# Performance work log

Hardware: AMD Instinct MI355X
Metric: run time of the kernel (lower is better)

## Reference

```python
import jax, jax.numpy as jnp
import numpy as np

N_NODES = 20000
K_RING = 8          # node i connects to i+1..i+K (mod n) -> degree 2K, E = N*K
D = 128
MH = 256


def _build_graph():
    n, k = N_NODES, K_RING
    i = np.arange(n, dtype=np.int64)
    # edges: eid = (j-1)*n + i  corresponds to edge (i, (i+j) % n)
    us, vs = [], []
    for j in range(1, k + 1):
        us.append(i)
        vs.append((i + j) % n)
    edges = np.stack([np.concatenate(us), np.concatenate(vs)], axis=1)  # [E,2]
    # triangle incidences: node t = (i+o)%n is adjacent to both endpoints of
    # edge (i, i+j) iff o in [j-k, k], o not in {0, j}
    tn, te = [], []
    for j in range(1, k + 1):
        eid = (j - 1) * n + i
        for o in range(j - k, k + 1):
            if o == 0 or o == j:
                continue
            tn.append((i + o) % n)
            te.append(eid)
    tri_node = np.concatenate(tn)  # [T], T = n * 84 for k=8
    tri_eid = np.concatenate(te)
    return edges, tri_node, tri_eid


def setup_inputs() -> dict:
    key = jax.random.key(0)
    ks = jax.random.split(key, 10)
    edges, tri_node, tri_eid = _build_graph()

    def w(k_, shape):
        fan_in = shape[0]
        return jax.random.normal(k_, shape, dtype=jnp.float32) * (1.0 / np.sqrt(fan_in))

    return {
        "h": jax.random.normal(ks[0], (N_NODES, D), dtype=jnp.float32),
        "edges": jnp.asarray(edges),
        "tri_node": jnp.asarray(tri_node),
        "tri_eid": jnp.asarray(tri_eid),
        "W_e1": w(ks[1], (D, MH)), "b_e1": jnp.zeros((MH,), jnp.float32),
        "W_e2": w(ks[2], (MH, D)), "b_e2": jnp.zeros((D,), jnp.float32),
        "W_f1": w(ks[3], (2 * D, MH)), "b_f1": jnp.zeros((MH,), jnp.float32),
        "W_f2": w(ks[4], (MH, D)), "b_f2": jnp.zeros((D,), jnp.float32),
        "W_r": w(ks[5], (D, D)), "b_r": jnp.zeros((D,), jnp.float32),
        "W_p1": w(ks[6], (D, MH)), "b_p1": jnp.zeros((MH,), jnp.float32),
        "W_p2": w(ks[7], (MH, D)), "b_p2": jnp.zeros((D,), jnp.float32),
    }


def _mlp(x, W1, b1, W2, b2):
    # 2-layer MLP, ReLU, dropout in eval mode (identity)
    return jnp.maximum(x @ W1 + b1, 0.0) @ W2 + b2


def reference(h, edges, tri_node, tri_eid,
              W_e1, b_e1, W_e2, b_e2,
              W_f1, b_f1, W_f2, b_f2,
              W_r, b_r, W_p1, b_p1, W_p2, b_p2):
    n = h.shape[0]
    u, v = edges[:, 0], edges[:, 1]
    h_e = _mlp(h[u] + h[v], W_e1, b_e1, W_e2, b_e2)          # [E,d]
    # aggr_t[t] = sum of h_e over edges incident to t
    ends = jnp.concatenate([u, v])
    aggr_t = jax.ops.segment_sum(jnp.concatenate([h_e, h_e], axis=0), ends,
                                 num_segments=n)               # [n,d]
    # aggr_n[t] = sum of h_e[eid] over neighbor-pair edges (triangles at t)
    aggr_n = jax.ops.segment_sum(h_e[tri_eid], tri_node, num_segments=n)
    z = _mlp(jnp.concatenate([aggr_t, aggr_n], axis=-1), W_f1, b_f1, W_f2, b_f2)
    deg = jax.ops.segment_sum(jnp.ones(ends.shape[0], h.dtype), ends,
                              num_segments=n)
    z = jnp.where((deg == 0)[:, None], 0.0, z)                 # isolated nodes
    h_new = _mlp(h @ W_r + b_r + z, W_p1, b_p1, W_p2, b_p2)    # lgan-res
    return h_new
```

## Files before the change

kernel.cpp:

```cpp
#include <hip/hip_runtime.h>


#define NN 20000
#define NE 160000
#define DD 128
#define MHD 256

typedef __attribute__((ext_vector_type(8))) short short8;
typedef __attribute__((ext_vector_type(4))) short short4v;
typedef __attribute__((ext_vector_type(4))) float f32x4;

#define SWZ(row) (((row) & 7) << 3)

__device__ __forceinline__ float bf2f(short s) {
  return __builtin_bit_cast(float, (unsigned int)((unsigned short)s) << 16);
}
__device__ __forceinline__ short f2bf(float f) {
  unsigned int u = __builtin_bit_cast(unsigned int, f);
  u = (u + 0x7FFFu + ((u >> 16) & 1u)) >> 16;
  return (short)u;
}
__device__ __forceinline__ short8 zero8() {
  short8 z;
#pragma unroll
  for (int q = 0; q < 8; ++q) z[q] = 0;
  return z;
}

#define MFMA(a, b, c) __builtin_amdgcn_mfma_f32_16x16x32_bf16((a), (b), (c), 0, 0, 0)

__global__ __launch_bounds__(256) void g_gemm(
    const short* __restrict__ hbf, const short* __restrict__ wqA,
    short* __restrict__ G) {
  __shared__ __align__(16) short WS[8192];
  const int t = threadIdx.x;
  const int lane = t & 63, w = t >> 6;
  const int lr = lane & 15, lg = lane >> 4;
  const int rbase = blockIdx.x * 128 + w * 32;

  short8 xf[2][4];
#pragma unroll
  for (int rs = 0; rs < 2; ++rs) {
    int r = rbase + rs * 16 + lr;
    if (r >= NN) r = NN - 1;
    const short* hr = hbf + (size_t)r * DD;
#pragma unroll
    for (int kk = 0; kk < 4; ++kk)
      xf[rs][kk] = *(const short8*)&hr[kk * 32 + lg * 8];
  }

#pragma unroll 1
  for (int p = 0; p < 4; ++p) {
    {
      short8 stg[4];
#pragma unroll
      for (int c = 0; c < 4; ++c)
        stg[c] = *(const short8*)&wqA[p * 8192 + (c * 256 + t) * 8];
#pragma unroll
      for (int c = 0; c < 4; ++c) *(short8*)&WS[(c * 256 + t) * 8] = stg[c];
    }
    __syncthreads();
#pragma unroll
    for (int ct = 0; ct < 4; ++ct) {
      short8 aw[4];
#pragma unroll
      for (int kk = 0; kk < 4; ++kk)
        aw[kk] = *(const short8*)&WS[(ct * 16 + lr) * 128 +
                                     (((kk * 4 + lg) ^ lr) << 3)];
#pragma unroll
      for (int rs = 0; rs < 2; ++rs) {
        f32x4 a1 = {0.f, 0.f, 0.f, 0.f};
#pragma unroll
        for (int kk = 0; kk < 4; ++kk) a1 = MFMA(aw[kk], xf[rs][kk], a1);
        const int row = rbase + rs * 16 + lr;
        if (row < NN) {
          short4v o;
#pragma unroll
          for (int q = 0; q < 4; ++q) o[q] = f2bf(a1[q]);
          const int off = p * 64 + ct * 16 + 4 * lg;
          *(short4v*)&G[(size_t)row * 256 + off] = o;
        }
      }
    }
    __syncthreads();
  }
}

#define LOADU(K, ridx)                                              \
  {                                                                 \
    int r_ = (ridx);                                                \
    if (r_ < 0) r_ += NN;                                           \
    else if (r_ >= NN) r_ -= NN;                                    \
    u##K = bf2f(G[(size_t)r_ * 256 + dbase]);                       \
  }

#define WIN(K)                                                          \
  ((K) == 0    ? u0                                                     \
   : (K) == 1  ? u1                                                     \
   : (K) == 2  ? u2                                                     \
   : (K) == 3  ? u3                                                     \
   : (K) == 4  ? u4                                                     \
   : (K) == 5  ? u5                                                     \
   : (K) == 6  ? u6                                                     \
   : (K) == 7  ? u7                                                     \
   : (K) == 8  ? u8                                                     \
   : (K) == 9  ? u9                                                     \
   : (K) == 10 ? u10                                                    \
   : (K) == 11 ? u11                                                    \
   : (K) == 12 ? u12                                                    \
   : (K) == 13 ? u13                                                    \
   : (K) == 14 ? u14                                                    \
   : (K) == 15 ? u15                                                    \
   : (K) == 16 ? u16                                                    \
   : (K) == 17 ? u17                                                    \
   : (K) == 18 ? u18                                                    \
   : (K) == 19 ? u19                                                    \
   : (K) == 20 ? u20                                                    \
   : (K) == 21 ? u21                                                    \
   : (K) == 22 ? u22                                                    \
   : (K) == 23 ? u23                                                    \
   : (K) == 24 ? u24                                                    \
   : (K) == 25 ? u25                                                    \
   : (K) == 26 ? u26                                                    \
   : (K) == 27 ? u27                                                    \
   : (K) == 28 ? u28                                                    \
   : (K) == 29 ? u29                                                    \
   : (K) == 30 ? u30                                                    \
   : (K) == 31 ? u31                                                    \
   : (K) == 32 ? u32                                                    \
   : (K) == 33 ? u33                                                    \
   : (K) == 34 ? u34                                                    \
   : (K) == 35 ? u35                                                    \
   : (K) == 36 ? u36                                                    \
   : (K) == 37 ? u37                                                    \
                : u38)

#define ADD16(base, W, v_)                                              \
  {                                                                     \
    constexpr int W__ = (W);                                            \
    if constexpr (W__ == 0) base##0 += (v_);                            \
    else if constexpr (W__ == 1) base##1 += (v_);                       \
    else if constexpr (W__ == 2) base##2 += (v_);                       \
    else if constexpr (W__ == 3) base##3 += (v_);                       \
    else if constexpr (W__ == 4) base##4 += (v_);                       \
    else if constexpr (W__ == 5) base##5 += (v_);                       \
    else if constexpr (W__ == 6) base##6 += (v_);                       \
    else if constexpr (W__ == 7) base##7 += (v_);                       \
    else if constexpr (W__ == 8) base##8 += (v_);                       \
    else if constexpr (W__ == 9) base##9 += (v_);                       \
    else if constexpr (W__ == 10) base##10 += (v_);                     \
    else if constexpr (W__ == 11) base##11 += (v_);                     \
    else if constexpr (W__ == 12) base##12 += (v_);                     \
    else if constexpr (W__ == 13) base##13 += (v_);                     \
    else if constexpr (W__ == 14) base##14 += (v_);                     \
    else if constexpr (W__ == 15) base##15 += (v_);                     \
  }

#define QJ(ii, j)                                                       \
  {                                                                     \
    float p = fmaxf(WIN((ii) + (j)) + gib, 0.f);                        \
    Q += p;                                                             \
    ADD16(sa, (ii) - 8 + (j), p)                                        \
    if constexpr ((j) <= 7) ADD16(sf, (ii) - 16 + (j), Q)               \
  }

#define PSTEP(ii)                                                       \
  {                                                                     \
    const float gib = WIN(ii) + b1v;                                    \
    float Q = 0.f;                                                      \
    QJ(ii, 1) QJ(ii, 2) QJ(ii, 3) QJ(ii, 4)                             \
    QJ(ii, 5) QJ(ii, 6) QJ(ii, 7) QJ(ii, 8)                             \
    ADD16(sa, (ii) - 8, Q)                                              \
    ADD16(sf, (ii) - 8, Q) ADD16(sf, (ii) - 7, Q) ADD16(sf, (ii) - 6, Q)\
    ADD16(sf, (ii) - 5, Q) ADD16(sf, (ii) - 4, Q) ADD16(sf, (ii) - 3, Q)\
    ADD16(sf, (ii) - 2, Q) ADD16(sf, (ii) - 1, Q) ADD16(sf, (ii) - 0, Q)\
  }

#define STORE_W(w_, saV, sfV)                                           \
  {                                                                     \
    SA[(size_t)(nb + (w_)) * 256 + sb] = f2bf(saV);                     \
    Dout[(size_t)(nb + (w_)) * 256 + sb] = f2bf(sfV - saV);             \
  }

__global__ __launch_bounds__(256) void paccum(
    const short* __restrict__ G, const float* __restrict__ be1,
    short* __restrict__ SA, short* __restrict__ Dout) {
  const int t = threadIdx.x;
  const int l = t & 63, wid = t >> 6;
  const int nb = blockIdx.x * 16;
  const int dbase = wid * 64 + l;
  const float b1v = be1[dbase];

  float u0, u1, u2, u3, u4, u5, u6, u7, u8, u9, u10, u11, u12, u13, u14,
      u15, u16, u17, u18, u19, u20, u21, u22, u23, u24, u25, u26, u27, u28,
      u29, u30, u31, u32, u33, u34, u35, u36, u37, u38;
  LOADU(0, nb - 8)  LOADU(1, nb - 7)  LOADU(2, nb - 6)  LOADU(3, nb - 5)
  LOADU(4, nb - 4)  LOADU(5, nb - 3)  LOADU(6, nb - 2)  LOADU(7, nb - 1)
  LOADU(8, nb)      LOADU(9, nb + 1)  LOADU(10, nb + 2) LOADU(11, nb + 3)
  LOADU(12, nb + 4) LOADU(13, nb + 5) LOADU(14, nb + 6) LOADU(15, nb + 7)
  LOADU(16, nb + 8) LOADU(17, nb + 9) LOADU(18, nb + 10) LOADU(19, nb + 11)
  LOADU(20, nb + 12) LOADU(21, nb + 13) LOADU(22, nb + 14) LOADU(23, nb + 15)
  LOADU(24, nb + 16) LOADU(25, nb + 17) LOADU(26, nb + 18) LOADU(27, nb + 19)
  LOADU(28, nb + 20) LOADU(29, nb + 21) LOADU(30, nb + 22) LOADU(31, nb + 23)
  LOADU(32, nb + 24) LOADU(33, nb + 25) LOADU(34, nb + 26) LOADU(35, nb + 27)
  LOADU(36, nb + 28) LOADU(37, nb + 29) LOADU(38, nb + 30)

  float sa0 = 0.f, sa1 = 0.f, sa2 = 0.f, sa3 = 0.f;
  float sa4 = 0.f, sa5 = 0.f, sa6 = 0.f, sa7 = 0.f;
  float sa8 = 0.f, sa9 = 0.f, sa10 = 0.f, sa11 = 0.f;
  float sa12 = 0.f, sa13 = 0.f, sa14 = 0.f, sa15 = 0.f;
  float sf0 = 0.f, sf1 = 0.f, sf2 = 0.f, sf3 = 0.f;
  float sf4 = 0.f, sf5 = 0.f, sf6 = 0.f, sf7 = 0.f;
  float sf8 = 0.f, sf9 = 0.f, sf10 = 0.f, sf11 = 0.f;
  float sf12 = 0.f, sf13 = 0.f, sf14 = 0.f, sf15 = 0.f;

  PSTEP(0)  PSTEP(1)  PSTEP(2)  PSTEP(3)  PSTEP(4)  PSTEP(5)
  PSTEP(6)  PSTEP(7)  PSTEP(8)  PSTEP(9)  PSTEP(10) PSTEP(11)
  PSTEP(12) PSTEP(13) PSTEP(14) PSTEP(15) PSTEP(16) PSTEP(17)
  PSTEP(18) PSTEP(19) PSTEP(20) PSTEP(21) PSTEP(22) PSTEP(23)
  PSTEP(24) PSTEP(25) PSTEP(26) PSTEP(27) PSTEP(28) PSTEP(29)
  PSTEP(30)

  const int sb = (dbase & ~31) | (((dbase >> 4) & 1) << 2) |
                 (((dbase >> 2) & 3) << 3) | (dbase & 3);
  STORE_W(0, sa0, sf0)   STORE_W(1, sa1, sf1)   STORE_W(2, sa2, sf2)
  STORE_W(3, sa3, sf3)   STORE_W(4, sa4, sf4)   STORE_W(5, sa5, sf5)
  STORE_W(6, sa6, sf6)   STORE_W(7, sa7, sf7)   STORE_W(8, sa8, sf8)
  STORE_W(9, sa9, sf9)   STORE_W(10, sa10, sf10) STORE_W(11, sa11, sf11)
  STORE_W(12, sa12, sf12) STORE_W(13, sa13, sf13) STORE_W(14, sa14, sf14)
  STORE_W(15, sa15, sf15)
}

__global__ __launch_bounds__(256) void catgemm(
    const short* __restrict__ SA, const short* __restrict__ Dm,
    const short* __restrict__ wqB, const float* __restrict__ be2,
    short* __restrict__ catb) {
  __shared__ __align__(16) short WS[8192];
  const int t = threadIdx.x;
  const int lane = t & 63, w = t >> 6;
  const int lr = lane & 15, lg = lane >> 4;
  const int vbase = blockIdx.x * 128 + w * 32;

  const short* srcp[2];
  int orow[2], dcb[2];
  float bm[2];
  bool ok[2];
#pragma unroll
  for (int rs = 0; rs < 2; ++rs) {
    int vr = vbase + rs * 16 + lr;
    ok[rs] = vr < 2 * NN;
    if (vr >= 2 * NN) vr = 2 * NN - 1;
    const bool isA = vr < NN;
    srcp[rs] = isA ? SA : Dm;
    orow[rs] = isA ? vr : vr - NN;
    bm[rs] = isA ? 16.0f : 84.0f;
    dcb[rs] = isA ? 0 : 128;
  }

  f32x4 acc[2][8];
#pragma unroll
  for (int rs = 0; rs < 2; ++rs)
#pragma unroll
    for (int ct2 = 0; ct2 < 8; ++ct2) acc[rs][ct2] = {0.f, 0.f, 0.f, 0.f};

#pragma unroll 1
  for (int p = 0; p < 4; ++p) {
    {
      short8 stg[4];
#pragma unroll
      for (int c = 0; c < 4; ++c)
        stg[c] = *(const short8*)&wqB[p * 8192 + (c * 256 + t) * 8];
#pragma unroll
      for (int c = 0; c < 4; ++c) *(short8*)&WS[(c * 256 + t) * 8] = stg[c];
    }
    __syncthreads();

    short8 pa[2][2];
#pragma unroll
    for (int rs = 0; rs < 2; ++rs)
#pragma unroll
      for (int kk2 = 0; kk2 < 2; ++kk2)
        pa[rs][kk2] = *(const short8*)&srcp[rs][(size_t)orow[rs] * 256 +
                                               p * 64 + kk2 * 32 + lg * 8];

#pragma unroll
    for (int kk2 = 0; kk2 < 2; ++kk2)
#pragma unroll
      for (int ct2 = 0; ct2 < 8; ++ct2) {
        short8 aw2 = *(const short8*)&WS[(ct2 * 16 + lr) * 64 +
                                         (((kk2 * 4 + lg) ^ (lr & 7)) << 3)];
        acc[0][ct2] = MFMA(aw2, pa[0][kk2], acc[0][ct2]);
        acc[1][ct2] = MFMA(aw2, pa[1][kk2], acc[1][ct2]);
      }
    __syncthreads();
  }

#pragma unroll
  for (int rs = 0; rs < 2; ++rs) {
    if (!ok[rs]) continue;
#pragma unroll
    for (int ct2 = 0; ct2 < 8; ++ct2) {
      const f32x4 bb = *(const f32x4*)&be2[ct2 * 16 + 4 * lg];
      short4v o;
#pragma unroll
      for (int q = 0; q < 4; ++q) o[q] = f2bf(acc[rs][ct2][q] + bm[rs] * bb[q]);
      *(short4v*)&catb[(size_t)orow[rs] * 256 + dcb[rs] + ct2 * 16 + 4 * lg] = o;
    }
  }
}

template <int NK, int LDX>
__device__ __forceinline__ void stage1s(const short* Xs, short* H1s,
                                        const short* __restrict__ W1t,
                                        const float* __restrict__ b1, int lane,
                                        int wid) {
  constexpr int K1 = NK * 32;
  const int lr = lane & 15, lg = lane >> 4;
#pragma unroll
  for (int ct = 0; ct < 4; ++ct) {
    const int wc = wid * 64 + ct * 16;
    short8 aw[NK];
#pragma unroll
    for (int kk = 0; kk < NK; ++kk)
      aw[kk] = *(const short8*)&W1t[(wc + lr) * K1 + kk * 32 + lg * 8];
    const f32x4 bias = *(const f32x4*)&b1[wc + 4 * lg];
#pragma unroll
    for (int r = 0; r < 4; ++r) {
      const int row = r * 16 + lr;
      const int swz = SWZ(row);
      short8 bx[NK];
#pragma unroll
      for (int kk = 0; kk < NK; ++kk)
        bx[kk] = *(const short8*)&Xs[row * LDX + ((kk * 32 + lg * 8) ^ swz)];
      f32x4 acc = bias;
#pragma unroll
      for (int kk = 0; kk < NK; ++kk) acc = MFMA(aw[kk], bx[kk], acc);
      short4v o;
#pragma unroll
      for (int q = 0; q < 4; ++q) {
        float v = acc[q] > 0.f ? acc[q] : 0.f;
        o[q] = f2bf(v);
      }
      *(short4v*)&H1s[row * 256 + ((wc + 4 * lg) ^ swz)] = o;
    }
  }
}

__device__ __forceinline__ void stage2s(const short* H1s,
                                        const short* __restrict__ W2t,
                                        f32x4 (&acc)[2][4], int lane, int wid) {
  const int lr = lane & 15, lg = lane >> 4;
#pragma unroll
  for (int ct = 0; ct < 2; ++ct) {
    const int wc = wid * 32 + ct * 16;
    short8 aw[8];
#pragma unroll
    for (int kk = 0; kk < 8; ++kk)
      aw[kk] = *(const short8*)&W2t[(wc + lr) * 256 + kk * 32 + lg * 8];
#pragma unroll
    for (int r = 0; r < 4; ++r) {
      const int row = r * 16 + lr;
      const int swz = SWZ(row);
#pragma unroll
      for (int kk = 0; kk < 8; ++kk) {
        short8 bh = *(const short8*)&H1s[row * 256 + ((kk * 32 + lg * 8) ^ swz)];
        acc[ct][r] = MFMA(aw[kk], bh, acc[ct][r]);
      }
    }
  }
}

__global__ __launch_bounds__(256) void fuse_out(
    const short* __restrict__ catb, const short* __restrict__ hbf,
    const short* __restrict__ Wf1t, const float* __restrict__ bf1,
    const short* __restrict__ Wf2t, const float* __restrict__ bf2,
    const short* __restrict__ Wrt, const float* __restrict__ br,
    const short* __restrict__ Wp1t, const float* __restrict__ bp1,
    const short* __restrict__ Wp2t, const float* __restrict__ bp2,
    float* __restrict__ out) {
  __shared__ __align__(16) short Xs[64][256];
  __shared__ __align__(16) short H1s[64][256];
  const int t = threadIdx.x;
  const int vbase = blockIdx.x * 64;
  {
    const int r = t >> 2, sub = t & 3;
    const int v = vbase + r;
    const bool valid = v < NN;
    const int swz = SWZ(r);
#pragma unroll
    for (int c = 0; c < 8; ++c) {
      const int d0 = sub * 64 + c * 8;
      short8 x = valid ? *(const short8*)&catb[(size_t)v * 256 + d0] : zero8();
      *(short8*)&Xs[r][d0 ^ swz] = x;
    }
  }
  __syncthreads();
  const int lane = t & 63, wid = t >> 6;
  stage1s<8, 256>(&Xs[0][0], &H1s[0][0], Wf1t, bf1, lane, wid);
  __syncthreads();
  const int lr = lane & 15, lg = lane >> 4;
  f32x4 acc[2][4];
#pragma unroll
  for (int ct = 0; ct < 2; ++ct) {
    const int wc = wid * 32 + ct * 16 + 4 * lg;
    f32x4 b0 = *(const f32x4*)&br[wc];
    f32x4 b1v = *(const f32x4*)&bf2[wc];
    f32x4 bias = b0 + b1v;
#pragma unroll
    for (int r = 0; r < 4; ++r) acc[ct][r] = bias;
  }
#pragma unroll
  for (int ct = 0; ct < 2; ++ct) {
    const int wc = wid * 32 + ct * 16;
    short8 aw[4];
#pragma unroll
    for (int kk = 0; kk < 4; ++kk)
      aw[kk] = *(const short8*)&Wrt[(wc + lr) * DD + kk * 32 + lg * 8];
#pragma unroll
    for (int r = 0; r < 4; ++r) {
      int v = vbase + r * 16 + lr;
      if (v >= NN) v = 0;
#pragma unroll
      for (int kk = 0; kk < 4; ++kk) {
        short8 bh = *(const short8*)&hbf[(size_t)v * DD + kk * 32 + lg * 8];
        acc[ct][r] = MFMA(aw[kk], bh, acc[ct][r]);
      }
    }
  }
  stage2s(&H1s[0][0], Wf2t, acc, lane, wid);

#pragma unroll
  for (int ct = 0; ct < 2; ++ct)
#pragma unroll
    for (int r = 0; r < 4; ++r) {
      const int row = r * 16 + lr;
      const int col = wid * 32 + ct * 16 + 4 * lg;
      short4v o;
#pragma unroll
      for (int q = 0; q < 4; ++q) o[q] = f2bf(acc[ct][r][q]);
      *(short4v*)&Xs[row][col ^ SWZ(row)] = o;
    }
  __syncthreads();

  stage1s<4, 256>(&Xs[0][0], &H1s[0][0], Wp1t, bp1, lane, wid);
  __syncthreads();
  f32x4 acc2[2][4];
#pragma unroll
  for (int ct = 0; ct < 2; ++ct) {
    const f32x4 bias = *(const f32x4*)&bp2[wid * 32 + ct * 16 + 4 * lg];
#pragma unroll
    for (int r = 0; r < 4; ++r) acc2[ct][r] = bias;
  }
  stage2s(&H1s[0][0], Wp2t, acc2, lane, wid);
#pragma unroll
  for (int ct = 0; ct < 2; ++ct)
#pragma unroll
    for (int r = 0; r < 4; ++r) {
      const int v = vbase + r * 16 + lr;
      if (v < NN)
        *(f32x4*)&out[(size_t)v * DD + wid * 32 + ct * 16 + 4 * lg] = acc2[ct][r];
    }
}

__global__ __launch_bounds__(256) void cvt_h(const float* __restrict__ src,
                                             short* __restrict__ dst) {
  const size_t id = (size_t)(blockIdx.x * 256 + threadIdx.x) * 8;
  float4 a = *(const float4*)&src[id];
  float4 b = *(const float4*)&src[id + 4];
  short8 o;
  o[0] = f2bf(a.x); o[1] = f2bf(a.y); o[2] = f2bf(a.z); o[3] = f2bf(a.w);
  o[4] = f2bf(b.x); o[5] = f2bf(b.y); o[6] = f2bf(b.z); o[7] = f2bf(b.w);
  *(short8*)&dst[id] = o;
}

__device__ __forceinline__ int klog_of_slot(int s) {
  return ((s >> 5) << 5) + (((s >> 2) & 1) << 4) + (((s >> 3) & 3) << 2) + (s & 3);
}

__global__ __launch_bounds__(256) void cvt_weights(
    const float* __restrict__ We1, const float* __restrict__ We2,
    const float* __restrict__ Wf1, const float* __restrict__ Wf2,
    const float* __restrict__ Wr, const float* __restrict__ Wp1,
    const float* __restrict__ Wp2, short* __restrict__ dst) {
  const int id = blockIdx.x * 256 + threadIdx.x;
  float v;
  if (id < 32768) {
    const int p = id >> 13, r = id & 8191;
    const int lm = r >> 7, e = r & 127;
    const int k = (((e >> 3) ^ (lm & 15)) << 3) | (e & 7);
    v = We1[k * 256 + p * 64 + lm];
  } else if (id < 65536) {
    const int l = id - 32768;
    const int p = l >> 13, i2 = l & 8191;
    const int o = i2 >> 6, e = i2 & 63;
    const int s = (((e >> 3) ^ (o & 7)) << 3) | (e & 7);
    v = We2[(p * 64 + klog_of_slot(s)) * 128 + o];
  } else if (id < 131072) {
    const int l = id - 65536;
    v = Wf1[(l & 255) * 256 + (l >> 8)];
  } else if (id < 163840) {
    const int l = id - 131072;
    v = Wf2[(l & 255) * 128 + (l >> 8)];
  } else if (id < 180224) {
    const int l = id - 163840;
    v = Wr[(l & 127) * 128 + (l >> 7)];
  } else if (id < 212992) {
    const int l = id - 180224;
    v = Wp1[(l & 127) * 256 + (l >> 7)];
  } else {
    const int l = id - 212992;
    v = Wp2[(l & 255) * 128 + (l >> 8)];
  }
  dst[id] = f2bf(v);
}

extern "C" void kernel_launch(void* const* d_in, const int* in_sizes, int n_in,
                              void* d_out, int out_size, void* d_ws,
                              size_t ws_size, hipStream_t stream) {
  const float* h = (const float*)d_in[0];
  const float* We1 = (const float*)d_in[4];
  const float* be1 = (const float*)d_in[5];
  const float* We2 = (const float*)d_in[6];
  const float* be2 = (const float*)d_in[7];
  const float* Wf1 = (const float*)d_in[8];
  const float* bf1 = (const float*)d_in[9];
  const float* Wf2 = (const float*)d_in[10];
  const float* bf2 = (const float*)d_in[11];
  const float* Wr = (const float*)d_in[12];
  const float* br = (const float*)d_in[13];
  const float* Wp1 = (const float*)d_in[14];
  const float* bp1 = (const float*)d_in[15];
  const float* Wp2 = (const float*)d_in[16];
  const float* bp2 = (const float*)d_in[17];

  char* ws = (char*)d_ws;
  short* hbf = (short*)ws;
  short* SA = (short*)(ws + 5120000);
  short* Dm = (short*)(ws + 15360000);
  short* catb = (short*)(ws + 46080000);
  short* wpool = (short*)(ws + 61440000);
  short* wqA = wpool;
  short* wqB = wpool + 32768;
  short* Wf1t = wpool + 65536;
  short* Wf2t = Wf1t + 65536;
  short* Wrt = Wf2t + 32768;
  short* Wp1t = Wrt + 16384;
  short* Wp2t = Wp1t + 32768;
  short* G = catb;

  cvt_h<<<1250, 256, 0, stream>>>(h, hbf);
  cvt_weights<<<960, 256, 0, stream>>>(We1, We2, Wf1, Wf2, Wr, Wp1, Wp2, wpool);
  g_gemm<<<(NN + 127) / 128, 256, 0, stream>>>(hbf, wqA, G);
  paccum<<<NN / 16, 256, 0, stream>>>(G, be1, SA, Dm);
  catgemm<<<(2 * NN + 127) / 128, 256, 0, stream>>>(SA, Dm, wqB, be2, catb);
  fuse_out<<<(NN + 63) / 64, 256, 0, stream>>>(catb, hbf, Wf1t, bf1, Wf2t, bf2,
                                               Wrt, br, Wp1t, bp1, Wp2t, bp2,
                                               (float*)d_out);
}
```

Measured before the change: 84.40 us.

## Fuse catgemm into fuse_out so concatenated features stay in shared memory

```diff
diff --git a/kernel.cpp b/kernel.cpp
--- a/kernel.cpp
+++ b/kernel.cpp
@@ -231,84 +231,6 @@
   STORE_W(15, sa15, sf15)
 }
 
-__global__ __launch_bounds__(256) void catgemm(
-    const short* __restrict__ SA, const short* __restrict__ Dm,
-    const short* __restrict__ wqB, const float* __restrict__ be2,
-    short* __restrict__ catb) {
-  __shared__ __align__(16) short WS[8192];
-  const int t = threadIdx.x;
-  const int lane = t & 63, w = t >> 6;
-  const int lr = lane & 15, lg = lane >> 4;
-  const int vbase = blockIdx.x * 128 + w * 32;
-
-  const short* srcp[2];
-  int orow[2], dcb[2];
-  float bm[2];
-  bool ok[2];
-#pragma unroll
-  for (int rs = 0; rs < 2; ++rs) {
-    int vr = vbase + rs * 16 + lr;
-    ok[rs] = vr < 2 * NN;
-    if (vr >= 2 * NN) vr = 2 * NN - 1;
-    const bool isA = vr < NN;
-    srcp[rs] = isA ? SA : Dm;
-    orow[rs] = isA ? vr : vr - NN;
-    bm[rs] = isA ? 16.0f : 84.0f;
-    dcb[rs] = isA ? 0 : 128;
-  }
-
-  f32x4 acc[2][8];
-#pragma unroll
-  for (int rs = 0; rs < 2; ++rs)
-#pragma unroll
-    for (int ct2 = 0; ct2 < 8; ++ct2) acc[rs][ct2] = {0.f, 0.f, 0.f, 0.f};
-
-#pragma unroll 1
-  for (int p = 0; p < 4; ++p) {
-    {
-      short8 stg[4];
-#pragma unroll
-      for (int c = 0; c < 4; ++c)
-        stg[c] = *(const short8*)&wqB[p * 8192 + (c * 256 + t) * 8];
-#pragma unroll
-      for (int c = 0; c < 4; ++c) *(short8*)&WS[(c * 256 + t) * 8] = stg[c];
-    }
-    __syncthreads();
-
-    short8 pa[2][2];
-#pragma unroll
-    for (int rs = 0; rs < 2; ++rs)
-#pragma unroll
-      for (int kk2 = 0; kk2 < 2; ++kk2)
-        pa[rs][kk2] = *(const short8*)&srcp[rs][(size_t)orow[rs] * 256 +
-                                               p * 64 + kk2 * 32 + lg * 8];
-
-#pragma unroll
-    for (int kk2 = 0; kk2 < 2; ++kk2)
-#pragma unroll
-      for (int ct2 = 0; ct2 < 8; ++ct2) {
-        short8 aw2 = *(const short8*)&WS[(ct2 * 16 + lr) * 64 +
-                                         (((kk2 * 4 + lg) ^ (lr & 7)) << 3)];
-        acc[0][ct2] = MFMA(aw2, pa[0][kk2], acc[0][ct2]);
-        acc[1][ct2] = MFMA(aw2, pa[1][kk2], acc[1][ct2]);
-      }
-    __syncthreads();
-  }
-
-#pragma unroll
-  for (int rs = 0; rs < 2; ++rs) {
-    if (!ok[rs]) continue;
-#pragma unroll
-    for (int ct2 = 0; ct2 < 8; ++ct2) {
-      const f32x4 bb = *(const f32x4*)&be2[ct2 * 16 + 4 * lg];
-      short4v o;
-#pragma unroll
-      for (int q = 0; q < 4; ++q) o[q] = f2bf(acc[rs][ct2][q] + bm[rs] * bb[q]);
-      *(short4v*)&catb[(size_t)orow[rs] * 256 + dcb[rs] + ct2 * 16 + 4 * lg] = o;
-    }
-  }
-}
-
 template <int NK, int LDX>
 __device__ __forceinline__ void stage1s(const short* Xs, short* H1s,
                                         const short* __restrict__ W1t,
@@ -370,35 +292,97 @@
   }
 }
 
-__global__ __launch_bounds__(256) void fuse_out(
-    const short* __restrict__ catb, const short* __restrict__ hbf,
-    const short* __restrict__ Wf1t, const float* __restrict__ bf1,
-    const short* __restrict__ Wf2t, const float* __restrict__ bf2,
-    const short* __restrict__ Wrt, const float* __restrict__ br,
-    const short* __restrict__ Wp1t, const float* __restrict__ bp1,
-    const short* __restrict__ Wp2t, const float* __restrict__ bp2,
-    float* __restrict__ out) {
+__global__ __launch_bounds__(256) void fuse_all(
+    const short* __restrict__ SA, const short* __restrict__ Dm,
+    const short* __restrict__ hbf, const short* __restrict__ wqB,
+    const float* __restrict__ be2, const short* __restrict__ Wf1t,
+    const float* __restrict__ bf1, const short* __restrict__ Wf2t,
+    const float* __restrict__ bf2, const short* __restrict__ Wrt,
+    const float* __restrict__ br, const short* __restrict__ Wp1t,
+    const float* __restrict__ bp1, const short* __restrict__ Wp2t,
+    const float* __restrict__ bp2, float* __restrict__ out) {
   __shared__ __align__(16) short Xs[64][256];
   __shared__ __align__(16) short H1s[64][256];
   const int t = threadIdx.x;
+  const int lane = t & 63, wid = t >> 6;
+  const int lr = lane & 15, lg = lane >> 4;
   const int vbase = blockIdx.x * 64;
+
   {
-    const int r = t >> 2, sub = t & 3;
-    const int v = vbase + r;
-    const bool valid = v < NN;
-    const int swz = SWZ(r);
-#pragma unroll
-    for (int c = 0; c < 8; ++c) {
-      const int d0 = sub * 64 + c * 8;
-      short8 x = valid ? *(const short8*)&catb[(size_t)v * 256 + d0] : zero8();
-      *(short8*)&Xs[r][d0 ^ swz] = x;
-    }
-  }
-  __syncthreads();
-  const int lane = t & 63, wid = t >> 6;
+    short* WSp = &H1s[0][0];
+    const short* srcp[2];
+    int orow[2], dcb[2], xrow[2];
+    float bm[2];
+#pragma unroll
+    for (int rs = 0; rs < 2; ++rs) {
+      const int vr = wid * 32 + rs * 16 + lr;
+      const bool isA = vr < 64;
+      xrow[rs] = vr & 63;
+      int node = vbase + xrow[rs];
+      if (node >= NN) node = NN - 1;
+      srcp[rs] = isA ? SA : Dm;
+      orow[rs] = node;
+      bm[rs] = isA ? 16.0f : 84.0f;
+      dcb[rs] = isA ? 0 : 128;
+    }
+
+    f32x4 acc[2][8];
+#pragma unroll
+    for (int rs = 0; rs < 2; ++rs)
+#pragma unroll
+      for (int ct2 = 0; ct2 < 8; ++ct2) acc[rs][ct2] = {0.f, 0.f, 0.f, 0.f};
+
+#pragma unroll 1
+    for (int p = 0; p < 4; ++p) {
+      {
+        short8 stg[4];
+#pragma unroll
+        for (int c = 0; c < 4; ++c)
+          stg[c] = *(const short8*)&wqB[p * 8192 + (c * 256 + t) * 8];
+#pragma unroll
+        for (int c = 0; c < 4; ++c) *(short8*)&WSp[(c * 256 + t) * 8] = stg[c];
+      }
+      __syncthreads();
+
+      short8 pa[2][2];
+#pragma unroll
+      for (int rs = 0; rs < 2; ++rs)
+#pragma unroll
+        for (int kk2 = 0; kk2 < 2; ++kk2)
+          pa[rs][kk2] = *(const short8*)&srcp[rs][(size_t)orow[rs] * 256 +
+                                                 p * 64 + kk2 * 32 + lg * 8];
+
+#pragma unroll
+      for (int kk2 = 0; kk2 < 2; ++kk2)
+#pragma unroll
+        for (int ct2 = 0; ct2 < 8; ++ct2) {
+          short8 aw2 = *(const short8*)&WSp[(ct2 * 16 + lr) * 64 +
+                                            (((kk2 * 4 + lg) ^ (lr & 7)) << 3)];
+          acc[0][ct2] = MFMA(aw2, pa[0][kk2], acc[0][ct2]);
+          acc[1][ct2] = MFMA(aw2, pa[1][kk2], acc[1][ct2]);
+        }
+      __syncthreads();
+    }
+
+#pragma unroll
+    for (int rs = 0; rs < 2; ++rs) {
+      const int row = xrow[rs];
+      const int swz = SWZ(row);
+#pragma unroll
+      for (int ct2 = 0; ct2 < 8; ++ct2) {
+        const f32x4 bb = *(const f32x4*)&be2[ct2 * 16 + 4 * lg];
+        short4v o;
+#pragma unroll
+        for (int q = 0; q < 4; ++q)
+          o[q] = f2bf(acc[rs][ct2][q] + bm[rs] * bb[q]);
+        *(short4v*)&Xs[row][(dcb[rs] + ct2 * 16 + 4 * lg) ^ swz] = o;
+      }
+    }
+    __syncthreads();
+  }
+
   stage1s<8, 256>(&Xs[0][0], &H1s[0][0], Wf1t, bf1, lane, wid);
   __syncthreads();
-  const int lr = lane & 15, lg = lane >> 4;
   f32x4 acc[2][4];
 #pragma unroll
   for (int ct = 0; ct < 2; ++ct) {
@@ -537,7 +521,7 @@
   short* hbf = (short*)ws;
   short* SA = (short*)(ws + 5120000);
   short* Dm = (short*)(ws + 15360000);
-  short* catb = (short*)(ws + 46080000);
+  short* G = (short*)(ws + 46080000);
   short* wpool = (short*)(ws + 61440000);
   short* wqA = wpool;
   short* wqB = wpool + 32768;
@@ -546,14 +530,12 @@
   short* Wrt = Wf2t + 32768;
   short* Wp1t = Wrt + 16384;
   short* Wp2t = Wp1t + 32768;
-  short* G = catb;
 
   cvt_h<<<1250, 256, 0, stream>>>(h, hbf);
   cvt_weights<<<960, 256, 0, stream>>>(We1, We2, Wf1, Wf2, Wr, Wp1, Wp2, wpool);
   g_gemm<<<(NN + 127) / 128, 256, 0, stream>>>(hbf, wqA, G);
   paccum<<<NN / 16, 256, 0, stream>>>(G, be1, SA, Dm);
-  catgemm<<<(2 * NN + 127) / 128, 256, 0, stream>>>(SA, Dm, wqB, be2, catb);
-  fuse_out<<<(NN + 63) / 64, 256, 0, stream>>>(catb, hbf, Wf1t, bf1, Wf2t, bf2,
-                                               Wrt, br, Wp1t, bp1, Wp2t, bp2,
-                                               (float*)d_out);
-}
+  fuse_all<<<(NN + 63) / 64, 256, 0, stream>>>(SA, Dm, hbf, wqB, be2, Wf1t,
+                                               bf1, Wf2t, bf2, Wrt, br, Wp1t,
+                                               bp1, Wp2t, bp2, (float*)d_out);
+}
```

After: 78.81 us. -6.6%, faster.
